# Kernel optimization log

Hardware: AMD Instinct MI355X
Metric: run time of the kernel (lower is better)

Reference implementation:

```python
import jax, jax.numpy as jnp
import numpy as np

NODES = 23   # 22 players + ball per frame-graph
K = 8        # random neighbors per node
B, T = 64, 128
G = B * T            # total graphs (frames)
N = G * NODES        # total nodes
D_IN, H, RH = 16, 128, 128


def setup_inputs() -> dict:
    key = jax.random.key(0)
    ks = jax.random.split(key, 10)
    x = jax.random.normal(ks[0], (N, D_IN), jnp.float32)
    # per-graph random edges: dst = each node repeated K times, src = random node in same graph
    src_local = jax.random.randint(ks[1], (G, NODES * K), 0, NODES)
    dst_local = jnp.tile(jnp.repeat(jnp.arange(NODES), K)[None, :], (G, 1))
    off = (jnp.arange(G) * NODES)[:, None]
    edge_index = jnp.stack([(src_local + off).reshape(-1),
                            (dst_local + off).reshape(-1)]).astype(jnp.int32)
    runner_idx = jax.random.randint(ks[2], (G,), 0, NODES, dtype=jnp.int32)
    sc = lambda k, sh: (jax.random.normal(k, sh, jnp.float32) * 0.05)
    return {
        'x': x, 'edge_index': edge_index, 'runner_idx': runner_idx,
        'W1': sc(ks[3], (D_IN, H)), 'b1': jnp.zeros((H,), jnp.float32),
        'W2': sc(ks[4], (H, H)),    'b2': jnp.zeros((H,), jnp.float32),
        'W_ih': sc(ks[5], (3 * RH, H)), 'W_hh': sc(ks[6], (3 * RH, RH)),
        'b_ih': jnp.zeros((3 * RH,), jnp.float32), 'b_hh': jnp.zeros((3 * RH,), jnp.float32),
        'Wp': sc(ks[7], (RH, 2)), 'bp': jnp.zeros((2,), jnp.float32),
    }


def _gcn_conv(h, edge_index, W, b):
    # PyG GCNConv: add self-loops, symmetric normalization, scatter-sum
    h = h @ W
    loop = jnp.arange(N, dtype=edge_index.dtype)
    s = jnp.concatenate([edge_index[0], loop])
    d = jnp.concatenate([edge_index[1], loop])
    deg = jax.ops.segment_sum(jnp.ones_like(s, h.dtype), d, num_segments=N)
    dinv = jnp.where(deg > 0, jax.lax.rsqrt(deg), 0.0)
    norm = dinv[s] * dinv[d]                      # [E+N]
    out = jax.ops.segment_sum(h[s] * norm[:, None], d, num_segments=N)
    return out + b


def _gru(seq, W_ih, W_hh, b_ih, b_hh):
    # torch GRU: gates in r,z,n order
    xg = seq @ W_ih.T + b_ih                      # [B,T,3RH]
    def step(hprev, xt):
        gh = hprev @ W_hh.T + b_hh
        xr, xz, xn = jnp.split(xt, 3, axis=-1)
        hr, hz, hn = jnp.split(gh, 3, axis=-1)
        r = jax.nn.sigmoid(xr + hr)
        z = jax.nn.sigmoid(xz + hz)
        n = jnp.tanh(xn + r * hn)
        hnew = (1.0 - z) * n + z * hprev
        return hnew, hnew
    h0 = jnp.zeros((seq.shape[0], RH), seq.dtype)
    _, outs = jax.lax.scan(step, h0, jnp.swapaxes(xg, 0, 1))
    return jnp.swapaxes(outs, 0, 1)               # [B,T,RH]


def reference(x, edge_index, runner_idx, W1, b1, W2, b2,
              W_ih, W_hh, b_ih, b_hh, Wp, bp):
    h = jax.nn.relu(_gcn_conv(x, edge_index, W1, b1))
    h = jax.nn.relu(_gcn_conv(h, edge_index, W2, b2))
    # fused equivalent of the per-graph nonzero()/indexing loop:
    runner_global = jnp.arange(G, dtype=jnp.int32) * NODES + runner_idx
    seq = h[runner_global].reshape(B, T, H)       # all lengths == T, padding is a no-op
    out = _gru(seq, W_ih, W_hh, b_ih, b_hh)
    return out @ Wp + bp                          # [B,T,2]
```

## Files before the change

kernel.cpp:

```cpp
#include <hip/hip_runtime.h>
#include <hip/hip_bf16.h>
#include <math.h>

#define GG 8192
#define NODESN 23
#define KK 8
#define DIN 16
#define HH 128
#define RHH 128
#define EPG (NODESN*KK)
#define TTT 128
#define BBB 64

template<int CTRL>
static __device__ __forceinline__ float dpp_add(float v) {
    int x = __builtin_amdgcn_update_dpp(0, __float_as_int(v), CTRL, 0xF, 0xF, true);
    return v + __int_as_float(x);
}
#define DPP_XOR1 0xB1
#define DPP_XOR2 0x4E
#define DPP_MIR7 0x141
#define DPP_SHL4 0x104

__global__ __launch_bounds__(256) void gcn_fused(
    const float* __restrict__ x, const int* __restrict__ esrc,
    const int* __restrict__ runner,
    const float* __restrict__ W1, const float* __restrict__ b1,
    const float* __restrict__ W2, const float* __restrict__ b2,
    float* __restrict__ seq)
{
    __shared__ float t1[4 * NODESN * HH];
    __shared__ int   srcs[4 * EPG];
    __shared__ float red4[4 * 256];
    __shared__ float hs[4 * HH];

    const int g0   = blockIdx.x * 4;
    const int tid  = threadIdx.x;
    const int j    = tid & 127;
    const int half = tid >> 7;

    for (int i = tid; i < 4 * EPG; i += 256) {
        int gg = i / EPG;
        srcs[i] = esrc[(size_t)g0 * EPG + i] - (g0 + gg) * NODESN;
    }

    float w[DIN];
    #pragma unroll
    for (int k = 0; k < DIN; k++) w[k] = W1[k * HH + j];
    const float b1j = b1[j];

    const int n0 = half ? 12 : 0;
    const int n1 = half ? NODESN : 12;
    for (int gg = 0; gg < 4; gg++) {
        const float* xgp = x + (size_t)(g0 + gg) * NODESN * DIN;
        for (int n = n0; n < n1; n++) {
            const float4* xr = (const float4*)(xgp + n * DIN);
            float4 a0 = xr[0], a1 = xr[1], a2 = xr[2], a3 = xr[3];
            float acc;
            acc = fmaf(a0.x, w[0],  fmaf(a0.y, w[1],  fmaf(a0.z, w[2],  fmaf(a0.w, w[3],
                  fmaf(a1.x, w[4],  fmaf(a1.y, w[5],  fmaf(a1.z, w[6],  fmaf(a1.w, w[7],
                  fmaf(a2.x, w[8],  fmaf(a2.y, w[9],  fmaf(a2.z, w[10], fmaf(a2.w, w[11],
                  fmaf(a3.x, w[12], fmaf(a3.y, w[13], fmaf(a3.z, w[14], fmaf(a3.w, w[15],
                  0.f))))))))))))))));
            t1[((gg * NODESN + n) << 7) + j] = acc;
        }
    }
    __syncthreads();

    for (int gg = 0; gg < 4; gg++) {
        const int r = runner[g0 + gg];
        const int* sg = srcs + gg * EPG;
        const float* tg = t1 + ((gg * NODESN) << 7);
        float part = 0.f;
        for (int slot = half; slot < 9; slot += 2) {
            int node = (slot < 8) ? sg[r * KK + slot] : r;
            float acc = tg[(node << 7) + j];
            #pragma unroll
            for (int k = 0; k < KK; k++) acc += tg[(sg[node * KK + k] << 7) + j];
            part += fmaxf(acc * (1.f / 9.f) + b1j, 0.f);
        }
        red4[gg * 256 + tid] = part;
    }
    __syncthreads();

    {
        int gg = tid >> 7, jj = tid & 127;
        hs[gg * HH + jj]       = red4[gg * 256 + jj]       + red4[gg * 256 + jj + 128];
        hs[(gg + 2) * HH + jj] = red4[(gg + 2) * 256 + jj] + red4[(gg + 2) * 256 + jj + 128];
    }
    __syncthreads();

    {
        const float b2j = b2[j];
        const float* h0 = hs + (half * 2) * HH;
        float acc0 = 0.f, acc1 = 0.f;
        for (int k = 0; k < HH; k += 4) {
            float w0  = W2[(k + 0) * HH + j];
            float w1  = W2[(k + 1) * HH + j];
            float w2v = W2[(k + 2) * HH + j];
            float w3  = W2[(k + 3) * HH + j];
            float4 hv0 = *(const float4*)(h0 + k);
            float4 hv1 = *(const float4*)(h0 + HH + k);
            acc0 = fmaf(hv0.x, w0, fmaf(hv0.y, w1, fmaf(hv0.z, w2v, fmaf(hv0.w, w3, acc0))));
            acc1 = fmaf(hv1.x, w0, fmaf(hv1.y, w1, fmaf(hv1.z, w2v, fmaf(hv1.w, w3, acc1))));
        }
        seq[(size_t)(g0 + half * 2 + 0) * HH + j] = fmaxf(acc0 * (1.f / 9.f) + b2j, 0.f);
        seq[(size_t)(g0 + half * 2 + 1) * HH + j] = fmaxf(acc1 * (1.f / 9.f) + b2j, 0.f);
    }
}

__global__ void transpose_wih(const float* __restrict__ W, float* __restrict__ WT)
{
    int idx = blockIdx.x * 256 + threadIdx.x;
    if (idx < 3 * RHH * RHH) {
        int jj = idx / RHH, kk = idx - jj * RHH;
        WT[kk * (3 * RHH) + jj] = W[idx];
    }
}

__global__ __launch_bounds__(384) void xg_kernel(
    const float* __restrict__ seq, const float* __restrict__ WT,
    const float* __restrict__ b_ih, float* __restrict__ xg)
{
    const int tid = threadIdx.x;
    const int m0 = blockIdx.x * 8;
    const float* srow = seq + (size_t)m0 * RHH;
    float acc[8];
    const float bv = b_ih[tid];
    #pragma unroll
    for (int mi = 0; mi < 8; mi++) acc[mi] = bv;
    for (int k = 0; k < RHH; k += 4) {
        float w0 = WT[(k+0)*384 + tid];
        float w1 = WT[(k+1)*384 + tid];
        float w2 = WT[(k+2)*384 + tid];
        float w3 = WT[(k+3)*384 + tid];
        #pragma unroll
        for (int mi = 0; mi < 8; mi++) {
            float4 sv = *(const float4*)(srow + mi * RHH + k);
            acc[mi] = fmaf(sv.x, w0, fmaf(sv.y, w1, fmaf(sv.z, w2, fmaf(sv.w, w3, acc[mi]))));
        }
    }
    #pragma unroll
    for (int mi = 0; mi < 8; mi++)
        xg[(size_t)(m0 + mi) * 384 + tid] = acc[mi];
}

#define CHUNK 32
#define XGB_FLOATS (CHUNK * HH * 4)

__global__ __launch_bounds__(512)
__attribute__((amdgpu_waves_per_eu(2, 2)))
void gru_kernel(
    const float* __restrict__ xg, const float* __restrict__ W_hh,
    const float* __restrict__ b_hh, const float* __restrict__ Wp,
    const float* __restrict__ bp, float* __restrict__ out)
{
    __shared__ float xgbuf[XGB_FLOATS];
    __shared__ float houtb[(CHUNK + 2) * HH];
    __shared__ float wps[2 * RHH + 2];

    const int b   = blockIdx.x;
    const int tid = threadIdx.x;
    const int kq  = tid & 7;
    const int i0  = tid >> 3;
    const int uhf = kq >> 2;
    const int u   = 2 * i0 + uhf;

    float4 wr0[4], wz0[4], wn0[4], wr1[4], wz1[4], wn1[4];
    int hof[4];
    {
        const float* w0 = W_hh + (size_t)(2 * i0) * RHH + kq * 16;
        #pragma unroll
        for (int m = 0; m < 4; m++) {
            const int off = 4 * ((m + kq) & 3);
            hof[m] = kq * 16 + off;
            wr0[m] = *(const float4*)(w0 + off);
            wz0[m] = *(const float4*)(w0 + RHH * RHH + off);
            wn0[m] = *(const float4*)(w0 + 2 * RHH * RHH + off);
            wr1[m] = *(const float4*)(w0 + RHH + off);
            wz1[m] = *(const float4*)(w0 + RHH * RHH + RHH + off);
            wn1[m] = *(const float4*)(w0 + 2 * RHH * RHH + RHH + off);
        }
    }
    const float bhr = b_hh[u];
    const float bhz = b_hh[RHH + u];
    const float bhn = b_hh[2 * RHH + u];

    if (tid < 2 * RHH) wps[tid] = Wp[tid];
    if (tid < 2)       wps[2 * RHH + tid] = bp[tid];
    if (tid < HH)      houtb[CHUNK * HH + tid] = 0.f;
    float hprev = 0.f;

    const float* xbase = xg + (size_t)b * TTT * 3 * RHH;
    float* outb = out + (size_t)b * TTT * 2;

    for (int c = 0; c < TTT / CHUNK; c++) {
        #pragma unroll
        for (int k2 = 0; k2 < 8; k2++) {
            int slot = tid + (k2 << 9);
            int tl = slot >> 7, ii = slot & 127;
            const float* gsrc = xbase + (size_t)(c * CHUNK + tl) * 384 + ii;
            float4 v;
            v.x = gsrc[0]; v.y = gsrc[128]; v.z = gsrc[256]; v.w = 0.f;
            *(float4*)&xgbuf[slot << 2] = v;
        }
        if (c > 0) {
            const int s  = tid & 7;
            const int cc = (tid >> 3) & 1;
            const int tl = tid >> 4;
            const float* hr = &houtb[(tl + 1) * HH + s * 16];
            float acc = 0.f;
            #pragma unroll
            for (int m = 0; m < 16; m += 4) {
                float4 hv = *(const float4*)(hr + m);
                int k = s * 16 + m;
                acc = fmaf(hv.x, wps[(k+0)*2 + cc],
                      fmaf(hv.y, wps[(k+1)*2 + cc],
                      fmaf(hv.z, wps[(k+2)*2 + cc],
                      fmaf(hv.w, wps[(k+3)*2 + cc], acc))));
            }
            acc = dpp_add<DPP_XOR1>(acc);
            acc = dpp_add<DPP_XOR2>(acc);
            acc = dpp_add<DPP_SHL4>(acc);
            if (s == 0)
                outb[((c - 1) * CHUNK + tl) * 2 + cc] = acc + wps[2 * RHH + cc];
        }
        __syncthreads();

        float4 xgv = *(const float4*)&xgbuf[u << 2];
        for (int tl = 0; tl < CHUNK; tl++) {
            const float* hrow = &houtb[(tl == 0 ? CHUNK : tl) * HH];
            float4 xgn = xgv;
            if (tl + 1 < CHUNK)
                xgn = *(const float4*)&xgbuf[((tl + 1) * HH + u) << 2];

            float ar0 = 0.f, az0 = 0.f, an0 = 0.f;
            float ar1 = 0.f, az1 = 0.f, an1 = 0.f;
            #pragma unroll
            for (int m = 0; m < 4; m++) {
                float4 hv = *(const float4*)(hrow + hof[m]);
                ar0 = fmaf(hv.x, wr0[m].x, fmaf(hv.y, wr0[m].y, fmaf(hv.z, wr0[m].z, fmaf(hv.w, wr0[m].w, ar0))));
                az0 = fmaf(hv.x, wz0[m].x, fmaf(hv.y, wz0[m].y, fmaf(hv.z, wz0[m].z, fmaf(hv.w, wz0[m].w, az0))));
                an0 = fmaf(hv.x, wn0[m].x, fmaf(hv.y, wn0[m].y, fmaf(hv.z, wn0[m].z, fmaf(hv.w, wn0[m].w, an0))));
                ar1 = fmaf(hv.x, wr1[m].x, fmaf(hv.y, wr1[m].y, fmaf(hv.z, wr1[m].z, fmaf(hv.w, wr1[m].w, ar1))));
                az1 = fmaf(hv.x, wz1[m].x, fmaf(hv.y, wz1[m].y, fmaf(hv.z, wz1[m].z, fmaf(hv.w, wz1[m].w, az1))));
                an1 = fmaf(hv.x, wn1[m].x, fmaf(hv.y, wn1[m].y, fmaf(hv.z, wn1[m].z, fmaf(hv.w, wn1[m].w, an1))));
            }
            ar0 = dpp_add<DPP_XOR1>(ar0); ar0 = dpp_add<DPP_XOR2>(ar0); ar0 = dpp_add<DPP_MIR7>(ar0);
            az0 = dpp_add<DPP_XOR1>(az0); az0 = dpp_add<DPP_XOR2>(az0); az0 = dpp_add<DPP_MIR7>(az0);
            an0 = dpp_add<DPP_XOR1>(an0); an0 = dpp_add<DPP_XOR2>(an0); an0 = dpp_add<DPP_MIR7>(an0);
            ar1 = dpp_add<DPP_XOR1>(ar1); ar1 = dpp_add<DPP_XOR2>(ar1); ar1 = dpp_add<DPP_MIR7>(ar1);
            az1 = dpp_add<DPP_XOR1>(az1); az1 = dpp_add<DPP_XOR2>(az1); az1 = dpp_add<DPP_MIR7>(az1);
            an1 = dpp_add<DPP_XOR1>(an1); an1 = dpp_add<DPP_XOR2>(an1); an1 = dpp_add<DPP_MIR7>(an1);

            float ar = uhf ? ar1 : ar0;
            float az = uhf ? az1 : az0;
            float an = uhf ? an1 : an0;

            float sr = xgv.x + ar + bhr;
            float sz = xgv.y + az + bhz;
            float rg = 1.f / (1.f + __expf(-sr));
            float zg = 1.f / (1.f + __expf(-sz));
            float tv = fmaf(rg, an + bhn, xgv.z);
            tv = fminf(fmaxf(tv, -15.f), 15.f);
            float e2 = __expf(-2.f * tv);
            float ng = (1.f - e2) / (1.f + e2);
            hprev = fmaf(zg, hprev, (1.f - zg) * ng);
            if ((kq & 3) == 0) houtb[(tl + 1) * HH + u] = hprev;
            xgv = xgn;
            __syncthreads();
        }
    }

    {
        const int s  = tid & 7;
        const int cc = (tid >> 3) & 1;
        const int tl = tid >> 4;
        const float* hr = &houtb[(tl + 1) * HH + s * 16];
        float acc = 0.f;
        #pragma unroll
        for (int m = 0; m < 16; m += 4) {
            float4 hv = *(const float4*)(hr + m);
            int k = s * 16 + m;
            acc = fmaf(hv.x, wps[(k+0)*2 + cc],
                  fmaf(hv.y, wps[(k+1)*2 + cc],
                  fmaf(hv.z, wps[(k+2)*2 + cc],
                  fmaf(hv.w, wps[(k+3)*2 + cc], acc))));
        }
        acc = dpp_add<DPP_XOR1>(acc);
        acc = dpp_add<DPP_XOR2>(acc);
        acc = dpp_add<DPP_SHL4>(acc);
        if (s == 0)
            outb[((TTT / CHUNK - 1) * CHUNK + tl) * 2 + cc] = acc + wps[2 * RHH + cc];
    }
}

extern "C" void kernel_launch(void* const* d_in, const int* in_sizes, int n_in,
                              void* d_out, int out_size, void* d_ws, size_t ws_size,
                              hipStream_t stream)
{
    const float* x      = (const float*)d_in[0];
    const int*   eidx   = (const int*)d_in[1];
    const int*   runner = (const int*)d_in[2];
    const float* W1     = (const float*)d_in[3];
    const float* b1     = (const float*)d_in[4];
    const float* W2     = (const float*)d_in[5];
    const float* b2     = (const float*)d_in[6];
    const float* W_ih   = (const float*)d_in[7];
    const float* W_hh   = (const float*)d_in[8];
    const float* b_ih   = (const float*)d_in[9];
    const float* b_hh   = (const float*)d_in[10];
    const float* Wp     = (const float*)d_in[11];
    const float* bp     = (const float*)d_in[12];
    float* out = (float*)d_out;

    float* seq = (float*)d_ws;
    float* xg  = seq + (size_t)GG * HH;
    float* WT  = xg + (size_t)GG * 3 * RHH;

    transpose_wih<<<192, 256, 0, stream>>>(W_ih, WT);
    gcn_fused<<<GG / 4, 256, 0, stream>>>(x, eidx, runner, W1, b1, W2, b2, seq);
    xg_kernel<<<GG / 8, 384, 0, stream>>>(seq, WT, b_ih, xg);
    gru_kernel<<<BBB, 512, 0, stream>>>(xg, W_hh, b_hh, Wp, bp, out);
}
```

Before: 289.5 us.

## Process one graph per GCN block and pin GRU weights in registers

The GCN kernel now handles one graph per block instead of four. Edge indices are read straight from global memory instead of staged in shared memory, and the W2 matvec is split over the two thread halves along K with a shared-memory reduction. This cuts shared memory per block and raises block count and occupancy, at the cost of reloading W1/W2 per graph and more blocks overall. Separately, empty asm constraints pin the GRU recurrent weight float4s in VGPRs so the compiler does not rematerialize or spill them inside the time loop.

```diff
diff --git a/kernel.cpp b/kernel.cpp
--- a/kernel.cpp
+++ b/kernel.cpp
@@ -22,90 +22,78 @@
 #define DPP_MIR7 0x141
 #define DPP_SHL4 0x104
 
-__global__ __launch_bounds__(256) void gcn_fused(
+#define PIN4(v4) asm volatile("" : "+v"((v4).x), "+v"((v4).y), "+v"((v4).z), "+v"((v4).w))
+
+__global__ __launch_bounds__(256) void gcn_seq(
     const float* __restrict__ x, const int* __restrict__ esrc,
     const int* __restrict__ runner,
     const float* __restrict__ W1, const float* __restrict__ b1,
     const float* __restrict__ W2, const float* __restrict__ b2,
     float* __restrict__ seq)
 {
-    __shared__ float t1[4 * NODESN * HH];
-    __shared__ int   srcs[4 * EPG];
-    __shared__ float red4[4 * 256];
-    __shared__ float hs[4 * HH];
-
-    const int g0   = blockIdx.x * 4;
-    const int tid  = threadIdx.x;
-    const int j    = tid & 127;
-    const int half = tid >> 7;
-
-    for (int i = tid; i < 4 * EPG; i += 256) {
-        int gg = i / EPG;
-        srcs[i] = esrc[(size_t)g0 * EPG + i] - (g0 + gg) * NODESN;
-    }
+    __shared__ float t1[NODESN * HH];
+    __shared__ float red[256];
+    __shared__ float hs[HH];
+
+    const int g   = blockIdx.x;
+    const int tid = threadIdx.x;
+    const int j   = tid & 127;
+    const int nhu = __builtin_amdgcn_readfirstlane(tid >> 7);
 
     float w[DIN];
     #pragma unroll
     for (int k = 0; k < DIN; k++) w[k] = W1[k * HH + j];
     const float b1j = b1[j];
 
-    const int n0 = half ? 12 : 0;
-    const int n1 = half ? NODESN : 12;
-    for (int gg = 0; gg < 4; gg++) {
-        const float* xgp = x + (size_t)(g0 + gg) * NODESN * DIN;
-        for (int n = n0; n < n1; n++) {
-            const float4* xr = (const float4*)(xgp + n * DIN);
-            float4 a0 = xr[0], a1 = xr[1], a2 = xr[2], a3 = xr[3];
-            float acc;
-            acc = fmaf(a0.x, w[0],  fmaf(a0.y, w[1],  fmaf(a0.z, w[2],  fmaf(a0.w, w[3],
-                  fmaf(a1.x, w[4],  fmaf(a1.y, w[5],  fmaf(a1.z, w[6],  fmaf(a1.w, w[7],
-                  fmaf(a2.x, w[8],  fmaf(a2.y, w[9],  fmaf(a2.z, w[10], fmaf(a2.w, w[11],
-                  fmaf(a3.x, w[12], fmaf(a3.y, w[13], fmaf(a3.z, w[14], fmaf(a3.w, w[15],
-                  0.f))))))))))))))));
-            t1[((gg * NODESN + n) << 7) + j] = acc;
-        }
+    const float* xgp = x + (size_t)g * NODESN * DIN;
+    const int n0 = nhu ? 12 : 0;
+    const int n1 = nhu ? NODESN : 12;
+    for (int n = n0; n < n1; n++) {
+        const float4* xr = (const float4*)(xgp + n * DIN);
+        float4 a0 = xr[0], a1 = xr[1], a2 = xr[2], a3 = xr[3];
+        float acc;
+        acc = fmaf(a0.x, w[0],  fmaf(a0.y, w[1],  fmaf(a0.z, w[2],  fmaf(a0.w, w[3],
+              fmaf(a1.x, w[4],  fmaf(a1.y, w[5],  fmaf(a1.z, w[6],  fmaf(a1.w, w[7],
+              fmaf(a2.x, w[8],  fmaf(a2.y, w[9],  fmaf(a2.z, w[10], fmaf(a2.w, w[11],
+              fmaf(a3.x, w[12], fmaf(a3.y, w[13], fmaf(a3.z, w[14], fmaf(a3.w, w[15],
+              0.f))))))))))))))));
+        t1[n * HH + j] = acc;
     }
     __syncthreads();
 
-    for (int gg = 0; gg < 4; gg++) {
-        const int r = runner[g0 + gg];
-        const int* sg = srcs + gg * EPG;
-        const float* tg = t1 + ((gg * NODESN) << 7);
-        float part = 0.f;
-        for (int slot = half; slot < 9; slot += 2) {
-            int node = (slot < 8) ? sg[r * KK + slot] : r;
-            float acc = tg[(node << 7) + j];
-            #pragma unroll
-            for (int k = 0; k < KK; k++) acc += tg[(sg[node * KK + k] << 7) + j];
-            part += fmaxf(acc * (1.f / 9.f) + b1j, 0.f);
-        }
-        red4[gg * 256 + tid] = part;
-    }
+    const int* eg = esrc + (size_t)g * EPG;
+    const int gb = g * NODESN;
+    const int r  = runner[g];
+    float part = 0.f;
+    for (int slot = nhu; slot < 9; slot += 2) {
+        int node = (slot < 8) ? (eg[r * KK + slot] - gb) : r;
+        float acc = t1[node * HH + j];
+        #pragma unroll
+        for (int k = 0; k < KK; k++) acc += t1[(eg[node * KK + k] - gb) * HH + j];
+        part += fmaxf(acc * (1.f / 9.f) + b1j, 0.f);
+    }
+    red[tid] = part;
     __syncthreads();
+    if (tid < HH) hs[tid] = red[tid] + red[tid + 128];
+    __syncthreads();
 
     {
-        int gg = tid >> 7, jj = tid & 127;
-        hs[gg * HH + jj]       = red4[gg * 256 + jj]       + red4[gg * 256 + jj + 128];
-        hs[(gg + 2) * HH + jj] = red4[(gg + 2) * 256 + jj] + red4[(gg + 2) * 256 + jj + 128];
-    }
-    __syncthreads();
-
-    {
-        const float b2j = b2[j];
-        const float* h0 = hs + (half * 2) * HH;
-        float acc0 = 0.f, acc1 = 0.f;
-        for (int k = 0; k < HH; k += 4) {
-            float w0  = W2[(k + 0) * HH + j];
-            float w1  = W2[(k + 1) * HH + j];
-            float w2v = W2[(k + 2) * HH + j];
-            float w3  = W2[(k + 3) * HH + j];
-            float4 hv0 = *(const float4*)(h0 + k);
-            float4 hv1 = *(const float4*)(h0 + HH + k);
-            acc0 = fmaf(hv0.x, w0, fmaf(hv0.y, w1, fmaf(hv0.z, w2v, fmaf(hv0.w, w3, acc0))));
-            acc1 = fmaf(hv1.x, w0, fmaf(hv1.y, w1, fmaf(hv1.z, w2v, fmaf(hv1.w, w3, acc1))));
-        }
-        seq[(size_t)(g0 + half * 2 + 0) * HH + j] = fmaxf(acc0 * (1.f / 9.f) + b2j, 0.f);
-        seq[(size_t)(g0 + half * 2 + 1) * HH + j] = fmaxf(acc1 * (1.f / 9.f) + b2j, 0.f);
+        const int k0 = nhu * 64;
+        float acc = 0.f;
+        #pragma unroll 4
+        for (int kk = 0; kk < 64; kk += 4) {
+            int k = k0 + kk;
+            float4 hv = *(const float4*)&hs[k];
+            acc = fmaf(hv.x, W2[(k + 0) * HH + j],
+                  fmaf(hv.y, W2[(k + 1) * HH + j],
+                  fmaf(hv.z, W2[(k + 2) * HH + j],
+                  fmaf(hv.w, W2[(k + 3) * HH + j], acc))));
+        }
+        red[tid] = acc;
+        __syncthreads();
+        if (tid < HH)
+            seq[(size_t)g * HH + tid] =
+                fmaxf((red[tid] + red[tid + 128]) * (1.f / 9.f) + b2[tid], 0.f);
     }
 }
 
@@ -181,6 +169,11 @@
             wz1[m] = *(const float4*)(w0 + RHH * RHH + RHH + off);
             wn1[m] = *(const float4*)(w0 + 2 * RHH * RHH + RHH + off);
         }
+    }
+    #pragma unroll
+    for (int m = 0; m < 4; m++) {
+        PIN4(wr0[m]); PIN4(wz0[m]); PIN4(wn0[m]);
+        PIN4(wr1[m]); PIN4(wz1[m]); PIN4(wn1[m]);
     }
     const float bhr = b_hh[u];
     const float bhz = b_hh[RHH + u];
@@ -319,7 +312,7 @@
     float* WT  = xg + (size_t)GG * 3 * RHH;
 
     transpose_wih<<<192, 256, 0, stream>>>(W_ih, WT);
-    gcn_fused<<<GG / 4, 256, 0, stream>>>(x, eidx, runner, W1, b1, W2, b2, seq);
+    gcn_seq<<<GG, 256, 0, stream>>>(x, eidx, runner, W1, b1, W2, b2, seq);
     xg_kernel<<<GG / 8, 384, 0, stream>>>(seq, WT, b_ih, xg);
     gru_kernel<<<BBB, 512, 0, stream>>>(xg, W_hh, b_hh, Wp, bp, out);
 }
```

New measurement: 242.9 us. 16.1% less time.
